# Optimization experiments

Hardware: AMD Instinct MI355X
Metric: run time of the kernel (lower is better)

## Reference

```python
import jax, jax.numpy as jnp
import numpy as np

B, L, D = 16, 1024, 768
MAX_MENTION_LEN = 10
NEG_INF = -jnp.inf


def _static_bounds_and_keep(L, max_len):
    # mention_bounds[s, e] = (s, e); keep pairs with e - s + 1 <= max_len
    s = np.arange(L)[:, None]
    e = np.arange(L)[None, :]
    keep = ((e - s + 1) <= max_len).reshape(-1)  # static bool (L*L,)
    bounds = np.stack([np.broadcast_to(s, (L, L)), np.broadcast_to(e, (L, L))], axis=-1).reshape(-1, 2)
    return bounds[keep], keep


def setup_inputs() -> dict:
    key = jax.random.key(0)
    k1, k2, k3 = jax.random.split(key, 3)
    bert_output = jax.random.normal(k1, (B, L, D), dtype=jnp.float32)
    # contiguous prefix mask (padded-batch style), lengths in [L//2, L]
    lengths = jax.random.randint(k2, (B,), L // 2, L + 1)
    input_mask = jnp.arange(L)[None, :] < lengths[:, None]  # (B, L) bool
    W = jax.random.normal(k3, (3, D), dtype=jnp.float32) * 0.02  # Linear(768, 3) weight
    b = jnp.zeros((3,), dtype=jnp.float32)
    return {"bert_output": bert_output, "input_mask": input_mask, "W": W, "b": b}


def reference(bert_output, input_mask, W, b):
    Bc, Lc, _ = bert_output.shape
    logits = jnp.einsum('bld,kd->blk', bert_output, W) + b  # (B, L, 3)
    start_lp = jnp.where(input_mask, logits[..., 0], NEG_INF)
    end_lp = jnp.where(input_mask, logits[..., 1], NEG_INF)
    mention_lp = jnp.where(input_mask, logits[..., 2], NEG_INF)

    # inclusive cumsum at end index e; exclusive cumsum at start index s
    incl = jnp.cumsum(mention_lp, axis=1)  # (B, L)
    excl = jnp.concatenate([jnp.zeros((Bc, 1), incl.dtype), incl[:, :-1]], axis=1)  # (B, L)

    # scores[b, s, e] = start[s] + end[e] + sum_{i=s..e} mention[i]
    scores = start_lp[:, :, None] + end_lp[:, None, :] + incl[:, None, :] - excl[:, :, None]

    s_idx = jnp.arange(Lc)[:, None]
    e_idx = jnp.arange(Lc)[None, :]
    sizes = e_idx - s_idx + 1  # (L, L)
    valid = (sizes > 0)[None, :, :] & input_mask[:, None, :]  # (B, L, L)
    scores = jnp.where(valid, scores, NEG_INF)  # also overwrites any NaN from inf arithmetic, as torch does

    scores = scores.reshape(Bc, Lc * Lc)
    bounds_np, keep = _static_bounds_and_keep(Lc, MAX_MENTION_LEN)  # static numpy
    scores = scores[:, keep]  # (B, K) with static K
    bounds = jnp.broadcast_to(jnp.asarray(bounds_np, dtype=jnp.int64)[None], (Bc, bounds_np.shape[0], 2))
    return scores, bounds
```

## Files before the change

### kernel.cpp

```cpp
#include <hip/hip_runtime.h>
#include <math.h>

#define B_      16
#define L_      1024
#define D_      768
#define MAXLEN  10
#define NKEEP     533971
#define S_BREAK   1014
#define OFF_BREAK 523731

#define NEG_SENTINEL (-1.0e30f)

typedef float f32x2 __attribute__((ext_vector_type(2)));

__device__ __forceinline__ int row_off(int s) {
    return (s < S_BREAK) ? ((s * (s + 19)) >> 1)
                         : OFF_BREAK + (s - S_BREAK) * L_;
}

__global__ __launch_bounds__(256) void k_logits(
    const float* __restrict__ X, const float* __restrict__ W,
    const float* __restrict__ bias,
    float* __restrict__ sArr, float* __restrict__ eArr, float* __restrict__ mArr)
{
    const int wave = threadIdx.x >> 6;
    const int lane = threadIdx.x & 63;
    const int row  = blockIdx.x * 4 + wave;
    const float4* x4 = (const float4*)(X + (size_t)row * D_);
    const float4* w0 = (const float4*)(W);
    const float4* w1 = (const float4*)(W + D_);
    const float4* w2 = (const float4*)(W + 2 * D_);
    float a0 = 0.f, a1 = 0.f, a2 = 0.f;
#pragma unroll
    for (int k = 0; k < 3; ++k) {
        const int f = lane + 64 * k;
        const float4 x = x4[f];
        float4 u = w0[f]; a0 += x.x*u.x + x.y*u.y + x.z*u.z + x.w*u.w;
        float4 v = w1[f]; a1 += x.x*v.x + x.y*v.y + x.z*v.z + x.w*v.w;
        float4 t = w2[f]; a2 += x.x*t.x + x.y*t.y + x.z*t.z + x.w*t.w;
    }
#pragma unroll
    for (int off = 32; off; off >>= 1) {
        a0 += __shfl_xor(a0, off, 64);
        a1 += __shfl_xor(a1, off, 64);
        a2 += __shfl_xor(a2, off, 64);
    }
    if (lane == 0) {
        sArr[row] = a0 + bias[0];
        eArr[row] = a1 + bias[1];
        mArr[row] = a2 + bias[2];
    }
}

__global__ __launch_bounds__(64) void k_scan(float* __restrict__ mArr)
{
    const int b = blockIdx.x, lane = threadIdx.x;
    float4* p = (float4*)(mArr + b * L_ + lane * 16);
    float x[16];
#pragma unroll
    for (int i = 0; i < 4; ++i) {
        const float4 v = p[i];
        x[4*i+0] = v.x; x[4*i+1] = v.y; x[4*i+2] = v.z; x[4*i+3] = v.w;
    }
#pragma unroll
    for (int i = 1; i < 16; ++i) x[i] += x[i-1];
    const float tot = x[15];
    float inc = tot;
#pragma unroll
    for (int off = 1; off < 64; off <<= 1) {
        const float t = __shfl_up(inc, off, 64);
        if (lane >= off) inc += t;
    }
    const float prefix = inc - tot;
#pragma unroll
    for (int i = 0; i < 4; ++i) {
        p[i] = make_float4(x[4*i+0] + prefix, x[4*i+1] + prefix,
                           x[4*i+2] + prefix, x[4*i+3] + prefix);
    }
}

__global__ __launch_bounds__(256) void k_pairs(
    const float* __restrict__ sArr, const float* __restrict__ eArr,
    const float* __restrict__ incl, const int* __restrict__ mask,
    float* __restrict__ outScores, f32x2* __restrict__ outBounds)
{
    const int idx = blockIdx.x * 256 + threadIdx.x;
    if (idx >= NKEEP) return;
    int s, e;
    if (idx >= OFF_BREAK) {
        const int r = idx - OFF_BREAK;
        s = S_BREAK + (r >> 10);
        e = r & (L_ - 1);
    } else {
        const float f = sqrtf((float)(8 * idx + 361));
        s = (int)((f - 19.0f) * 0.5f);
        while (row_off(s + 1) <= idx) ++s;
        while (row_off(s) > idx) --s;
        e = idx - row_off(s);
    }
    f32x2 bnd; bnd.x = (float)s; bnd.y = (float)e;
    const bool ege = (e >= s);
#pragma unroll
    for (int b = 0; b < B_; ++b) {
        const bool valid = ege && (mask[b * L_ + e] != 0);
        const float slog = sArr[b * L_ + s];
        const float excl = (s > 0) ? incl[b * L_ + s - 1] : 0.0f;
        const float v = ((slog + eArr[b * L_ + e]) + incl[b * L_ + e]) - excl;
        const size_t o = (size_t)b * NKEEP + idx;
        outScores[o] = valid ? v : NEG_SENTINEL;
        outBounds[o] = bnd;
    }
}

extern "C" void kernel_launch(void* const* d_in, const int* in_sizes, int n_in,
                              void* d_out, int out_size, void* d_ws, size_t ws_size,
                              hipStream_t stream)
{
    const float* X    = (const float*)d_in[0];
    const int*   mask = (const int*)d_in[1];
    const float* W    = (const float*)d_in[2];
    const float* bias = (const float*)d_in[3];

    float* sArr = (float*)d_ws;
    float* eArr = sArr + B_ * L_;
    float* mArr = eArr + B_ * L_;

    float* outScores = (float*)d_out;
    f32x2* outBounds = (f32x2*)((char*)d_out +
                                (size_t)B_ * NKEEP * sizeof(float));

    hipLaunchKernelGGL(k_logits, dim3(B_ * L_ / 4), dim3(256), 0, stream,
                       X, W, bias, sArr, eArr, mArr);
    hipLaunchKernelGGL(k_scan, dim3(B_), dim3(64), 0, stream, mArr);
    hipLaunchKernelGGL(k_pairs, dim3((NKEEP + 255) / 256), dim3(256), 0, stream,
                       sArr, eArr, mArr, mask, outScores, outBounds);
}
```

Before: 161.8 us.

## Flatten pair kernel over batch and write four outputs per thread vectorized

The pair-score kernel now indexes the flattened (batch, pair) space. Each thread produces four consecutive outputs, walking (s, e) incrementally and wrapping across batch boundaries, then writes scores as one 16-byte store and bounds as two 16-byte stores. The goal is wider, fully coalesced writes for the large output and fewer per-thread sqrt-based index decodes. The cost is a division per thread and a sequential stepping loop. It relies on TOT being divisible by 4 and on aligned vector stores.

```diff
diff --git a/kernel.cpp b/kernel.cpp
--- a/kernel.cpp
+++ b/kernel.cpp
@@ -8,10 +8,12 @@
 #define NKEEP     533971
 #define S_BREAK   1014
 #define OFF_BREAK 523731
+#define TOT       (B_ * NKEEP)
 
 #define NEG_SENTINEL (-1.0e30f)
 
 typedef float f32x2 __attribute__((ext_vector_type(2)));
+typedef float f32x4 __attribute__((ext_vector_type(4)));
 
 __device__ __forceinline__ int row_off(int s) {
     return (s < S_BREAK) ? ((s * (s + 19)) >> 1)
@@ -84,32 +86,50 @@
     const float* __restrict__ incl, const int* __restrict__ mask,
     float* __restrict__ outScores, f32x2* __restrict__ outBounds)
 {
-    const int idx = blockIdx.x * 256 + threadIdx.x;
-    if (idx >= NKEEP) return;
+    const uint32_t g0 = (blockIdx.x * 256u + threadIdx.x) * 4u;
+    if (g0 >= (uint32_t)TOT) return;
+    uint32_t b   = g0 / (uint32_t)NKEEP;
+    uint32_t idx = g0 - b * (uint32_t)NKEEP;
     int s, e;
     if (idx >= OFF_BREAK) {
-        const int r = idx - OFF_BREAK;
-        s = S_BREAK + (r >> 10);
-        e = r & (L_ - 1);
+        const uint32_t r = idx - OFF_BREAK;
+        s = S_BREAK + (int)(r >> 10);
+        e = (int)(r & (L_ - 1));
     } else {
-        const float f = sqrtf((float)(8 * idx + 361));
+        const float f = sqrtf((float)(8u * idx + 361u));
         s = (int)((f - 19.0f) * 0.5f);
-        while (row_off(s + 1) <= idx) ++s;
-        while (row_off(s) > idx) --s;
-        e = idx - row_off(s);
+        while (row_off(s + 1) <= (int)idx) ++s;
+        while (row_off(s) > (int)idx) --s;
+        e = (int)idx - row_off(s);
     }
-    f32x2 bnd; bnd.x = (float)s; bnd.y = (float)e;
-    const bool ege = (e >= s);
+    int cs = min(s + MAXLEN, L_);
+
+    float sc[4];
+    float bs[4], be[4];
 #pragma unroll
-    for (int b = 0; b < B_; ++b) {
-        const bool valid = ege && (mask[b * L_ + e] != 0);
-        const float slog = sArr[b * L_ + s];
-        const float excl = (s > 0) ? incl[b * L_ + s - 1] : 0.0f;
-        const float v = ((slog + eArr[b * L_ + e]) + incl[b * L_ + e]) - excl;
-        const size_t o = (size_t)b * NKEEP + idx;
-        outScores[o] = valid ? v : NEG_SENTINEL;
-        outBounds[o] = bnd;
+    for (int j = 0; j < 4; ++j) {
+        if (j) {
+            ++idx;
+            if (idx == (uint32_t)NKEEP) {
+                idx = 0; ++b; s = 0; e = 0; cs = MAXLEN;
+            } else {
+                ++e;
+                if (e == cs) { ++s; e = 0; cs = min(s + MAXLEN, L_); }
+            }
+        }
+        const int base = (int)b * L_;
+        const bool valid = (e >= s) && (mask[base + e] != 0);
+        const float excl = (s > 0) ? incl[base + s - 1] : 0.0f;
+        const float v = ((sArr[base + s] + eArr[base + e]) + incl[base + e]) - excl;
+        sc[j] = valid ? v : NEG_SENTINEL;
+        bs[j] = (float)s; be[j] = (float)e;
     }
+    f32x4 sv; sv.x = sc[0]; sv.y = sc[1]; sv.z = sc[2]; sv.w = sc[3];
+    *(f32x4*)(outScores + g0) = sv;
+    f32x4 b0; b0.x = bs[0]; b0.y = be[0]; b0.z = bs[1]; b0.w = be[1];
+    f32x4 b1; b1.x = bs[2]; b1.y = be[2]; b1.z = bs[3]; b1.w = be[3];
+    f32x4* bp = (f32x4*)(outBounds + g0);
+    bp[0] = b0; bp[1] = b1;
 }
 
 extern "C" void kernel_launch(void* const* d_in, const int* in_sizes, int n_in,
@@ -132,6 +152,6 @@
     hipLaunchKernelGGL(k_logits, dim3(B_ * L_ / 4), dim3(256), 0, stream,
                        X, W, bias, sArr, eArr, mArr);
     hipLaunchKernelGGL(k_scan, dim3(B_), dim3(64), 0, stream, mArr);
-    hipLaunchKernelGGL(k_pairs, dim3((NKEEP + 255) / 256), dim3(256), 0, stream,
+    hipLaunchKernelGGL(k_pairs, dim3((TOT / 4 + 255) / 256), dim3(256), 0, stream,
                        sArr, eArr, mArr, mask, outScores, outBounds);
 }
```

Result: no change. 162.7 us (+0.5%).
